# Optimization experiments

Measured on AMD Instinct MI355X. Metric: run time of the kernel, lower is better.

## Reference

```python
import jax, jax.numpy as jnp
import numpy as np

# irreps layout: list of (multiplicity, l); input == hidden == 128x0e+64x1e+32x2e
IRREPS = [(128, 0), (64, 1), (32, 2)]
EPS = 1e-5


def _split(x, irreps):
    """Split flat [N, dim] into per-irrep fields [N, mul, 2l+1]."""
    fields, ix = [], 0
    for mul, l in irreps:
        d = 2 * l + 1
        fields.append(x[:, ix:ix + mul * d].reshape(-1, mul, d))
        ix += mul * d
    return fields


def _equiv_layernorm(x, w, b):
    """Equivariant layer norm (Equiformer-style): per-irrep RMS over (mul, comp),
    mean-subtraction + bias only for scalars; affine weight per multiplicity."""
    outs, iw = [], 0
    for (mul, l), f in zip(IRREPS, _split(x, IRREPS)):
        if l == 0:
            f = f - f.mean(axis=1, keepdims=True)
        norm2 = (f * f).sum(-1).mean(axis=1)          # [N]
        inv = jax.lax.rsqrt(norm2 + EPS)              # [N]
        f = f * (inv[:, None] * w[iw:iw + mul][None, :])[:, :, None]
        if l == 0:
            f = f + b[None, :, None]
        iw += mul
        outs.append(f.reshape(f.shape[0], -1))
    return jnp.concatenate(outs, axis=1)


def _o3_linear(fields, Ws):
    """Per-irrep linear with e3nn path normalization 1/sqrt(fan_in)."""
    return [jnp.einsum('nui,uv->nvi', f, W) / np.float32(np.sqrt(f.shape[1]))
            for f, W in zip(fields, Ws)]


def _gate(fields):
    """XequiNet Gate: sigmoid of per-channel invariant norm multiplies the channel."""
    out = []
    for f in fields:
        n = jnp.sqrt((f * f).sum(-1) + 1e-12)         # [N, mul]
        out.append(f * jax.nn.sigmoid(n)[..., None])
    return out


def setup_inputs() -> dict:
    key = jax.random.key(0)
    ks = jax.random.split(key, 8)
    N, B = 300000, 512
    atom_out = jax.random.normal(ks[0], (N, 480), dtype=jnp.float32)
    coords = jax.random.normal(ks[1], (N, 3), dtype=jnp.float32)
    at_no = jax.random.randint(ks[2], (N,), 0, 100, dtype=jnp.int64)
    batch_idx = jnp.sort(jax.random.randint(ks[3], (N,), 0, B, dtype=jnp.int64))
    return {
        'atom_out': atom_out,
        'coords': coords,
        'ln_w': jnp.ones((224,), jnp.float32),
        'ln_b': jnp.zeros((128,), jnp.float32),
        'W1_0': jax.random.normal(ks[4], (128, 128), dtype=jnp.float32),
        'W1_1': jax.random.normal(ks[5], (64, 64), dtype=jnp.float32),
        'W1_2': jax.random.normal(ks[6], (32, 32), dtype=jnp.float32),
        'W2': jax.random.normal(ks[7], (64, 1), dtype=jnp.float32),
        'at_no': at_no,
        'batch_idx': batch_idx,
        'num_graphs': B,
    }


def reference(atom_out, coords, ln_w, ln_b, W1_0, W1_1, W1_2, W2, at_no, batch_idx, num_graphs):
    x = _equiv_layernorm(atom_out, ln_w, ln_b)
    fields = _split(x, IRREPS)
    fields = _o3_linear(fields, [W1_0, W1_1, W1_2])
    fields = _gate(fields)
    # second o3.Linear to 1x1e: only the 1e block contributes
    vec = jnp.einsum('nui,uv->nvi', fields[1], W2) / np.float32(np.sqrt(64.0))  # [N,1,3]
    atom_res = vec[:, 0, :][:, jnp.array([2, 0, 1])]  # e3nn (y,z,x) -> (x,y,z)
    return jax.ops.segment_sum(atom_res, batch_idx, num_segments=num_graphs)
```

## Files before the change

kernel.cpp:

```cpp
#include <hip/hip_runtime.h>
#include <hip/hip_bf16.h>

#define WPB 2
#define BLOCK (WPB * 64)
#define GRID 768

typedef __attribute__((ext_vector_type(8))) short s16x8;
typedef __attribute__((ext_vector_type(4))) float f32x4;

#define GLL16(gp, lp) __builtin_amdgcn_global_load_lds( \
    (const __attribute__((address_space(1))) void*)(gp), \
    (__attribute__((address_space(3))) void*)(lp), 16, 0, 0)

__device__ __forceinline__ float wave_sum64(float v) {
#pragma unroll
    for (int m = 32; m >= 1; m >>= 1) v += __shfl_xor(v, m, 64);
    return v;
}

__device__ __forceinline__ short bf16b(float x) {
    union { float f; unsigned u; } c; c.f = x;
    unsigned r = c.u + 0x7FFFu + ((c.u >> 16) & 1u);
    return (short)(r >> 16);
}

__global__ __launch_bounds__(BLOCK, 2) void vecout_mfma(
    const float* __restrict__ atom_out,
    const float* __restrict__ ln_w,
    const float* __restrict__ W1_1,
    const float* __restrict__ W2,
    const int*   __restrict__ batch_idx,
    float* __restrict__ out,
    int N)
{
    __shared__ __align__(16) char Ash[WPB][2][12288];
    __shared__ float invsh[WPB][16];

    const int lane  = threadIdx.x & 63;
    const int wid   = threadIdx.x >> 6;
    const int col   = lane & 15;
    const int kgrp  = lane >> 4;
    const int atomi = lane & 15;

    const int NG  = (N + 15) >> 4;
    const int NW  = gridDim.x * WPB;
    const int w   = blockIdx.x * WPB + wid;
    const int cpw = NG / NW, rem = NG % NW;
    const int g0  = w * cpw + min(w, rem);
    const int cnt = cpw + (w < rem ? 1 : 0);
    if (cnt <= 0) return;
    const int gend = g0 + cnt;

    s16x8 Bf[2][4];
#pragma unroll
    for (int kt = 0; kt < 2; ++kt)
#pragma unroll
        for (int nt = 0; nt < 4; ++nt) {
            s16x8 b;
#pragma unroll
            for (int j = 0; j < 8; ++j) {
                int k = kt * 32 + kgrp * 8 + j;
                float wgt = W1_1[k * 64 + nt * 16 + col] * ln_w[128 + k] * 0.125f;
                b[j] = bf16b(wgt);
            }
            Bf[kt][nt] = b;
        }
    float w2r[4];
#pragma unroll
    for (int nt = 0; nt < 4; ++nt) w2r[nt] = W2[nt * 16 + col] * 0.125f;

    int prec[12];
#pragma unroll
    for (int c = 0; c < 12; ++c) {
        int P   = c * 1024 + lane * 16;
        int row = P / 768;
        int L   = P ^ ((row & 7) << 4);
        prec[c] = row * 1920 + 512 + (L - row * 768);
    }

    const char* gb = (const char*)atom_out;
    const unsigned key   = (unsigned)(atomi & 7) << 4;
    const unsigned base0 = (unsigned)(atomi * 768 + kgrp * 96);

    float acc[4][3];
#pragma unroll
    for (int r = 0; r < 4; ++r) { acc[r][0] = 0.f; acc[r][1] = 0.f; acc[r][2] = 0.f; }
    int accb = batch_idx[g0 * 16];

    auto flushAcc = [&]() {
        float s0 = acc[0][0] + acc[1][0] + acc[2][0] + acc[3][0];
        float s1 = acc[0][1] + acc[1][1] + acc[2][1] + acc[3][1];
        float s2 = acc[0][2] + acc[1][2] + acc[2][2] + acc[3][2];
        s0 = wave_sum64(s0); s1 = wave_sum64(s1); s2 = wave_sum64(s2);
        if (lane == 0) {
            atomicAdd(&out[accb * 3 + 0], s2);
            atomicAdd(&out[accb * 3 + 1], s0);
            atomicAdd(&out[accb * 3 + 2], s1);
        }
#pragma unroll
        for (int r = 0; r < 4; ++r) { acc[r][0] = 0.f; acc[r][1] = 0.f; acc[r][2] = 0.f; }
    };

    auto issueG = [&](int g, int buf) {
        char* Ab = &Ash[wid][buf][0];
        if (((g + 1) << 4) <= N) {
            const char* p = gb + (size_t)g * 30720;
#pragma unroll
            for (int c = 0; c < 12; ++c)
                GLL16(p + prec[c], Ab + c * 1024);
        } else {
#pragma unroll
            for (int c = 0; c < 12; ++c) {
                int P   = c * 1024 + lane * 16;
                int row = P / 768;
                int off = (P ^ ((row & 7) << 4)) - row * 768;
                int ga  = min(g * 16 + row, N - 1);
                GLL16(gb + (size_t)ga * 1920 + 512 + off, Ab + c * 1024);
            }
        }
    };

    issueG(g0, 0);
    if (g0 + 1 < gend) issueG(g0 + 1, 1);

    for (int g = g0; g < gend; ++g) {
        const int cur = (g - g0) & 1;
        const int a   = g * 16;
        const bool has_next = (g + 1 < gend);

        if (has_next) asm volatile("s_waitcnt vmcnt(12)" ::: "memory");
        else          asm volatile("s_waitcnt vmcnt(0)"  ::: "memory");

        char* Ab = &Ash[wid][cur][0];

        float F[48];
#pragma unroll
        for (int kt = 0; kt < 2; ++kt)
#pragma unroll
            for (int s = 0; s < 6; ++s) {
                unsigned ad = (base0 + (unsigned)(kt * 384 + s * 16)) ^ key;
                f32x4 t = *(const f32x4*)(Ab + ad);
                int i = (kt * 6 + s) * 4;
                F[i + 0] = t[0]; F[i + 1] = t[1]; F[i + 2] = t[2]; F[i + 3] = t[3];
            }
        asm volatile("s_waitcnt lgkmcnt(0)" ::: "memory");

        if (g + 2 < gend) issueG(g + 2, cur);

        float nrm = 0.f;
#pragma unroll
        for (int i = 0; i < 48; ++i) nrm += F[i] * F[i];
        nrm += __shfl_xor(nrm, 16, 64);
        nrm += __shfl_xor(nrm, 32, 64);
        float inv = rsqrtf(nrm * (1.0f / 64.0f) + 1e-5f);
        if (lane < 16) invsh[wid][lane] = inv;

        s16x8 Af[3][2];
#pragma unroll
        for (int c = 0; c < 3; ++c)
#pragma unroll
            for (int kt = 0; kt < 2; ++kt) {
                s16x8 fr;
#pragma unroll
                for (int j = 0; j < 8; ++j) fr[j] = bf16b(F[kt * 24 + 3 * j + c]);
                Af[c][kt] = fr;
            }

        f32x4 Cf[3][4];
#pragma unroll
        for (int c = 0; c < 3; ++c)
#pragma unroll
            for (int nt = 0; nt < 4; ++nt) {
                f32x4 z = {0.f, 0.f, 0.f, 0.f};
                z = __builtin_amdgcn_mfma_f32_16x16x32_bf16(Af[c][0], Bf[0][nt], z, 0, 0, 0);
                z = __builtin_amdgcn_mfma_f32_16x16x32_bf16(Af[c][1], Bf[1][nt], z, 0, 0, 0);
                Cf[c][nt] = z;
            }

        float invA[4];
#pragma unroll
        for (int r = 0; r < 4; ++r) invA[r] = invsh[wid][kgrp * 4 + r];

        float part[4][3];
#pragma unroll
        for (int r = 0; r < 4; ++r) {
            part[r][0] = 0.f; part[r][1] = 0.f; part[r][2] = 0.f;
            float iv = invA[r];
#pragma unroll
            for (int nt = 0; nt < 4; ++nt) {
                float g0v = Cf[0][nt][r] * iv;
                float g1v = Cf[1][nt][r] * iv;
                float g2v = Cf[2][nt][r] * iv;
                float q  = g0v * g0v + g1v * g1v + g2v * g2v;
                float nr = sqrtf(q + 1e-12f);
                float sg = 1.f / (1.f + __expf(-nr));
                float t  = sg * w2r[nt];
                part[r][0] += g0v * t; part[r][1] += g1v * t; part[r][2] += g2v * t;
            }
            if (a + kgrp * 4 + r >= N) { part[r][0] = 0.f; part[r][1] = 0.f; part[r][2] = 0.f; }
        }

        int bfst = batch_idx[a];
        int blst = batch_idx[min(a + 15, N - 1)];
        if (bfst == blst) {
            if (bfst != accb) { flushAcc(); accb = bfst; }
#pragma unroll
            for (int r = 0; r < 4; ++r) {
                acc[r][0] += part[r][0]; acc[r][1] += part[r][1]; acc[r][2] += part[r][2];
            }
        } else {
            flushAcc();
#pragma unroll
            for (int r = 0; r < 4; ++r) {
                float c0 = part[r][0], c1 = part[r][1], c2 = part[r][2];
#pragma unroll
                for (int m = 1; m < 16; m <<= 1) {
                    c0 += __shfl_xor(c0, m, 64);
                    c1 += __shfl_xor(c1, m, 64);
                    c2 += __shfl_xor(c2, m, 64);
                }
                int ai = a + kgrp * 4 + r;
                if (col == 0 && ai < N) {
                    int b = batch_idx[ai];
                    atomicAdd(&out[b * 3 + 0], c2);
                    atomicAdd(&out[b * 3 + 1], c0);
                    atomicAdd(&out[b * 3 + 2], c1);
                }
            }
            accb = blst;
        }
    }

    flushAcc();
}

extern "C" void kernel_launch(void* const* d_in, const int* in_sizes, int n_in,
                              void* d_out, int out_size, void* d_ws, size_t ws_size,
                              hipStream_t stream) {
    const float* atom_out  = (const float*)d_in[0];
    const float* ln_w      = (const float*)d_in[2];
    const float* W1_1      = (const float*)d_in[5];
    const float* W2        = (const float*)d_in[7];
    const int*   batch_idx = (const int*)d_in[9];
    float* out = (float*)d_out;

    const int N = in_sizes[0] / 480;

    hipMemsetAsync(d_out, 0, (size_t)out_size * sizeof(float), stream);

    vecout_mfma<<<GRID, BLOCK, 0, stream>>>(atom_out, ln_w, W1_1, W2, batch_idx, out, N);
}
```

Measured before the change: 70.93 us.

## Restructure inner loop: inline LDS reads, shuffle inv norms, interleave MFMA with gate

Reads LDS tiles with inline ds_read_b128 and converts them to bf16 fragments as they arrive, accumulating the norm in the same pass. Per-atom inverse norms are broadcast with wave shuffles instead of a shared-memory round trip. MFMAs are issued per output tile and interleaved with the gate math. The next-tile prefetch moves to the end of the iteration, and batch_idx loads use scalar (readfirstlane) addresses. The aim is lower register pressure and LDS traffic and better overlap, but the later prefetch shortens the time available to hide memory latency.

```diff
diff --git a/kernel.cpp b/kernel.cpp
--- a/kernel.cpp
+++ b/kernel.cpp
@@ -22,6 +22,12 @@
     union { float f; unsigned u; } c; c.f = x;
     unsigned r = c.u + 0x7FFFu + ((c.u >> 16) & 1u);
     return (short)(r >> 16);
+}
+
+__device__ __forceinline__ f32x4 lds_read_b128(unsigned addr) {
+    f32x4 r;
+    asm volatile("ds_read_b128 %0, %1" : "=v"(r) : "v"(addr));
+    return r;
 }
 
 __global__ __launch_bounds__(BLOCK, 2) void vecout_mfma(
@@ -34,13 +40,17 @@
     int N)
 {
     __shared__ __align__(16) char Ash[WPB][2][12288];
-    __shared__ float invsh[WPB][16];
 
     const int lane  = threadIdx.x & 63;
     const int wid   = threadIdx.x >> 6;
     const int col   = lane & 15;
     const int kgrp  = lane >> 4;
     const int atomi = lane & 15;
+    const unsigned key   = (unsigned)(atomi & 7) << 4;
+    const unsigned base0 = (unsigned)(atomi * 768 + kgrp * 96);
+
+    const unsigned ab0 = (unsigned)(size_t)
+        (__attribute__((address_space(3))) char*)&Ash[wid][0][0];
 
     const int NG  = (N + 15) >> 4;
     const int NW  = gridDim.x * WPB;
@@ -79,13 +89,11 @@
     }
 
     const char* gb = (const char*)atom_out;
-    const unsigned key   = (unsigned)(atomi & 7) << 4;
-    const unsigned base0 = (unsigned)(atomi * 768 + kgrp * 96);
 
     float acc[4][3];
 #pragma unroll
     for (int r = 0; r < 4; ++r) { acc[r][0] = 0.f; acc[r][1] = 0.f; acc[r][2] = 0.f; }
-    int accb = batch_idx[g0 * 16];
+    int accb = batch_idx[__builtin_amdgcn_readfirstlane(g0 * 16)];
 
     auto flushAcc = [&]() {
         float s0 = acc[0][0] + acc[1][0] + acc[2][0] + acc[3][0];
@@ -126,82 +134,74 @@
     for (int g = g0; g < gend; ++g) {
         const int cur = (g - g0) & 1;
         const int a   = g * 16;
-        const bool has_next = (g + 1 < gend);
-
-        if (has_next) asm volatile("s_waitcnt vmcnt(12)" ::: "memory");
-        else          asm volatile("s_waitcnt vmcnt(0)"  ::: "memory");
-
-        char* Ab = &Ash[wid][cur][0];
-
-        float F[48];
-#pragma unroll
-        for (int kt = 0; kt < 2; ++kt)
+
+        if (g + 1 < gend) asm volatile("s_waitcnt vmcnt(12)" ::: "memory");
+        else              asm volatile("s_waitcnt vmcnt(0)"  ::: "memory");
+        __builtin_amdgcn_sched_barrier(0);
+
+        const unsigned abase = ab0 + (unsigned)cur * 12288u;
+
+        float nrm = 0.f;
+        s16x8 Af[3][2];
+#pragma unroll
+        for (int kt = 0; kt < 2; ++kt) {
+            f32x4 V[6];
 #pragma unroll
             for (int s = 0; s < 6; ++s) {
-                unsigned ad = (base0 + (unsigned)(kt * 384 + s * 16)) ^ key;
-                f32x4 t = *(const f32x4*)(Ab + ad);
-                int i = (kt * 6 + s) * 4;
-                F[i + 0] = t[0]; F[i + 1] = t[1]; F[i + 2] = t[2]; F[i + 3] = t[3];
-            }
-        asm volatile("s_waitcnt lgkmcnt(0)" ::: "memory");
-
-        if (g + 2 < gend) issueG(g + 2, cur);
-
-        float nrm = 0.f;
-#pragma unroll
-        for (int i = 0; i < 48; ++i) nrm += F[i] * F[i];
+                unsigned ad = abase + ((base0 + (unsigned)(kt * 384 + s * 16)) ^ key);
+                V[s] = lds_read_b128(ad);
+            }
+            asm volatile("s_waitcnt lgkmcnt(0)" ::: "memory");
+            __builtin_amdgcn_sched_barrier(0);
+#pragma unroll
+            for (int s = 0; s < 6; ++s)
+#pragma unroll
+                for (int q = 0; q < 4; ++q) {
+                    int d = s * 4 + q;
+                    float v = V[s][q];
+                    nrm += v * v;
+                    Af[d % 3][kt][d / 3] = bf16b(v);
+                }
+        }
+
         nrm += __shfl_xor(nrm, 16, 64);
         nrm += __shfl_xor(nrm, 32, 64);
         float inv = rsqrtf(nrm * (1.0f / 64.0f) + 1e-5f);
-        if (lane < 16) invsh[wid][lane] = inv;
-
-        s16x8 Af[3][2];
-#pragma unroll
-        for (int c = 0; c < 3; ++c)
-#pragma unroll
-            for (int kt = 0; kt < 2; ++kt) {
-                s16x8 fr;
-#pragma unroll
-                for (int j = 0; j < 8; ++j) fr[j] = bf16b(F[kt * 24 + 3 * j + c]);
-                Af[c][kt] = fr;
-            }
-
-        f32x4 Cf[3][4];
-#pragma unroll
-        for (int c = 0; c < 3; ++c)
-#pragma unroll
-            for (int nt = 0; nt < 4; ++nt) {
-                f32x4 z = {0.f, 0.f, 0.f, 0.f};
-                z = __builtin_amdgcn_mfma_f32_16x16x32_bf16(Af[c][0], Bf[0][nt], z, 0, 0, 0);
-                z = __builtin_amdgcn_mfma_f32_16x16x32_bf16(Af[c][1], Bf[1][nt], z, 0, 0, 0);
-                Cf[c][nt] = z;
-            }
-
         float invA[4];
 #pragma unroll
-        for (int r = 0; r < 4; ++r) invA[r] = invsh[wid][kgrp * 4 + r];
+        for (int r = 0; r < 4; ++r) invA[r] = __shfl(inv, kgrp * 4 + r, 64);
 
         float part[4][3];
 #pragma unroll
-        for (int r = 0; r < 4; ++r) {
-            part[r][0] = 0.f; part[r][1] = 0.f; part[r][2] = 0.f;
-            float iv = invA[r];
-#pragma unroll
-            for (int nt = 0; nt < 4; ++nt) {
-                float g0v = Cf[0][nt][r] * iv;
-                float g1v = Cf[1][nt][r] * iv;
-                float g2v = Cf[2][nt][r] * iv;
+        for (int r = 0; r < 4; ++r) { part[r][0] = 0.f; part[r][1] = 0.f; part[r][2] = 0.f; }
+#pragma unroll
+        for (int nt = 0; nt < 4; ++nt) {
+            f32x4 C0 = {0.f,0.f,0.f,0.f}, C1 = {0.f,0.f,0.f,0.f}, C2 = {0.f,0.f,0.f,0.f};
+            C0 = __builtin_amdgcn_mfma_f32_16x16x32_bf16(Af[0][0], Bf[0][nt], C0, 0, 0, 0);
+            C0 = __builtin_amdgcn_mfma_f32_16x16x32_bf16(Af[0][1], Bf[1][nt], C0, 0, 0, 0);
+            C1 = __builtin_amdgcn_mfma_f32_16x16x32_bf16(Af[1][0], Bf[0][nt], C1, 0, 0, 0);
+            C1 = __builtin_amdgcn_mfma_f32_16x16x32_bf16(Af[1][1], Bf[1][nt], C1, 0, 0, 0);
+            C2 = __builtin_amdgcn_mfma_f32_16x16x32_bf16(Af[2][0], Bf[0][nt], C2, 0, 0, 0);
+            C2 = __builtin_amdgcn_mfma_f32_16x16x32_bf16(Af[2][1], Bf[1][nt], C2, 0, 0, 0);
+#pragma unroll
+            for (int r = 0; r < 4; ++r) {
+                float iv  = invA[r];
+                float g0v = C0[r] * iv;
+                float g1v = C1[r] * iv;
+                float g2v = C2[r] * iv;
                 float q  = g0v * g0v + g1v * g1v + g2v * g2v;
                 float nr = sqrtf(q + 1e-12f);
                 float sg = 1.f / (1.f + __expf(-nr));
                 float t  = sg * w2r[nt];
                 part[r][0] += g0v * t; part[r][1] += g1v * t; part[r][2] += g2v * t;
             }
+        }
+#pragma unroll
+        for (int r = 0; r < 4; ++r)
             if (a + kgrp * 4 + r >= N) { part[r][0] = 0.f; part[r][1] = 0.f; part[r][2] = 0.f; }
-        }
-
-        int bfst = batch_idx[a];
-        int blst = batch_idx[min(a + 15, N - 1)];
+
+        int bfst = batch_idx[__builtin_amdgcn_readfirstlane(a)];
+        int blst = batch_idx[__builtin_amdgcn_readfirstlane(min(a + 15, N - 1))];
         if (bfst == blst) {
             if (bfst != accb) { flushAcc(); accb = bfst; }
 #pragma unroll
@@ -229,6 +229,8 @@
             }
             accb = blst;
         }
+
+        if (g + 2 < gend) issueG(g + 2, cur);
     }
 
     flushAcc();
```

Result: no change. 70.04 us (-1.3%).
